# Performance work log

Hardware: AMD Instinct MI355X
Metric: run time of the kernel (lower is better)

## Reference

```python
import jax, jax.numpy as jnp
import numpy as np

B, L, S, D_MODEL, H = 2, 2048, 2048, 1024, 16
D_HEAD = D_MODEL // H  # 64


def setup_inputs() -> dict:
    key = jax.random.key(0)
    ks = jax.random.split(key, 11)
    s = 0.02
    return {
        "queries": jax.random.normal(ks[0], (B, L, D_MODEL), jnp.float32),
        "keys": jax.random.normal(ks[1], (B, S, D_MODEL), jnp.float32),
        "values": jax.random.normal(ks[2], (B, S, D_MODEL), jnp.float32),
        # Linear weights stored as [in, out] (torch W.T), biases [out]
        "Wq": jax.random.normal(ks[3], (D_MODEL, H * D_HEAD), jnp.float32) * s,
        "bq": jnp.zeros((H * D_HEAD,), jnp.float32),
        "Wk": jax.random.normal(ks[4], (D_MODEL, H * D_HEAD), jnp.float32) * s,
        "bk": jnp.zeros((H * D_HEAD,), jnp.float32),
        "Wv": jax.random.normal(ks[5], (D_MODEL, H * D_HEAD), jnp.float32) * s,
        "bv": jnp.zeros((H * D_HEAD,), jnp.float32),
        "Wo": jax.random.normal(ks[6], (H * D_HEAD, D_MODEL), jnp.float32) * s,
        "bo": jnp.zeros((D_MODEL,), jnp.float32),
    }


def reference(queries, keys, values, Wq, bq, Wk, bk, Wv, bv, Wo, bo):
    b, l, _ = queries.shape
    _, s, _ = keys.shape
    # QKV projections -> [B, L/S, H, D_HEAD]
    q = (queries @ Wq + bq).reshape(b, l, H, D_HEAD)
    k = (keys @ Wk + bk).reshape(b, s, H, D_HEAD)
    v = (values @ Wv + bv).reshape(b, s, H, D_HEAD)
    scale = 1.0 / jnp.sqrt(jnp.asarray(D_HEAD, q.dtype))
    # Full score matrix [B, H, L, S] (mask_flag=False -> no causal mask)
    scores = jnp.einsum("blhe,bshe->bhls", q, k)
    A = jax.nn.softmax(scale * scores, axis=-1)  # dropout is identity at eval
    out = jnp.einsum("bhls,bshd->blhd", A, v).reshape(b, l, H * D_HEAD)
    out = out @ Wo + bo
    return out, A
```

## Files before the change

### kernel.cpp

```cpp
#include <hip/hip_runtime.h>


typedef __attribute__((ext_vector_type(8))) __bf16 bf16x8;
typedef __attribute__((ext_vector_type(4))) float f32x4;

__device__ __forceinline__ unsigned int f2bf_u(float f) {
  unsigned int u = __float_as_uint(f);
  return (u + 0x7FFFu + ((u >> 16) & 1u)) >> 16;
}
__device__ __forceinline__ float bf2f(unsigned int h) {
  return __uint_as_float(h << 16);
}
__device__ __forceinline__ unsigned int pack2(float lo, float hi) {
  return (f2bf_u(hi) << 16) | f2bf_u(lo);
}
__device__ __forceinline__ f32x4 mfma16(bf16x8 a, bf16x8 b, f32x4 c) {
  return __builtin_amdgcn_mfma_f32_16x16x32_bf16(a, b, c, 0, 0, 0);
}
__device__ __forceinline__ void gll16(const void* g, void* l) {
  __builtin_amdgcn_global_load_lds(
      (const __attribute__((address_space(1))) unsigned int*)g,
      (__attribute__((address_space(3))) unsigned int*)l, 16, 0, 0);
}

__global__ __launch_bounds__(256) void transpose_w(
    const float* __restrict__ W0, const float* __restrict__ W1,
    const float* __restrict__ W2, const float* __restrict__ W3,
    unsigned short* __restrict__ T0, unsigned short* __restrict__ T1,
    unsigned short* __restrict__ T2, unsigned short* __restrict__ T3) {
  const float* W; unsigned short* T;
  switch (blockIdx.z) {
    case 0: W = W0; T = T0; break;
    case 1: W = W1; T = T1; break;
    case 2: W = W2; T = T2; break;
    default: W = W3; T = T3; break;
  }
  __shared__ float tile[32][33];
  const int tx = threadIdx.x, ty = threadIdx.y;
  const int i0 = blockIdx.x * 32, o0 = blockIdx.y * 32;
  #pragma unroll
  for (int r = 0; r < 4; ++r)
    tile[ty + 8 * r][tx] = W[(size_t)(i0 + ty + 8 * r) * 1024 + o0 + tx];
  __syncthreads();
  #pragma unroll
  for (int r = 0; r < 4; ++r)
    T[(size_t)(o0 + ty + 8 * r) * 1024 + i0 + tx] =
        (unsigned short)f2bf_u(tile[tx][ty + 8 * r]);
}

struct GemmJob {
  const float* A;
  const unsigned short* BT;
  const float* bias;
  void* C;
  int omode;
};
struct GemmJobs { GemmJob j[3]; };

__global__ __launch_bounds__(256) void gemm_qkv(GemmJobs jobs, int M, int N, int K) {
  const GemmJob jb = jobs.j[blockIdx.z];
  __shared__ unsigned short As[128][40];
  __shared__ unsigned short Bs[128][32];
  const int tid = threadIdx.x;
  const int lane = tid & 63, wid = tid >> 6;
  const int l15 = lane & 15, l4 = lane >> 4;
  const int m0 = blockIdx.x * 128, n0 = blockIdx.y * 128;
  const int wr = wid >> 1, wc = wid & 1;

  f32x4 acc[4][4];
  #pragma unroll
  for (int i = 0; i < 4; ++i)
    #pragma unroll
    for (int j = 0; j < 4; ++j) acc[i][j] = (f32x4){0.f, 0.f, 0.f, 0.f};

  const int nk = K >> 5;
  for (int kt = 0; kt < nk; ++kt) {
    #pragma unroll
    for (int c = 0; c < 4; ++c) {
      const int chunk = c * 256 + tid;
      const int row = chunk >> 3, col4 = chunk & 7;
      const float4 f = *(const float4*)(jb.A +
                                        (size_t)(m0 + row) * K + kt * 32 + col4 * 4);
      ushort4 o;
      o.x = (unsigned short)f2bf_u(f.x);
      o.y = (unsigned short)f2bf_u(f.y);
      o.z = (unsigned short)f2bf_u(f.z);
      o.w = (unsigned short)f2bf_u(f.w);
      *(ushort4*)&As[row][col4 * 4] = o;
    }
    #pragma unroll
    for (int c = 0; c < 2; ++c) {
      const int off = wid * 2048 + c * 1024;
      const int loff = off + lane * 16;
      const int row = loff >> 6, colb = loff & 63;
      gll16(jb.BT + (size_t)(n0 + row) * K + kt * 32 + colb / 2,
            (char*)&Bs[0][0] + off);
    }
    __syncthreads();
    bf16x8 af[4], bfr[4];
    #pragma unroll
    for (int i = 0; i < 4; ++i)
      af[i] = *(const bf16x8*)&As[wr * 64 + i * 16 + l15][l4 * 8];
    #pragma unroll
    for (int j = 0; j < 4; ++j)
      bfr[j] = *(const bf16x8*)&Bs[wc * 64 + j * 16 + l15][l4 * 8];
    #pragma unroll
    for (int i = 0; i < 4; ++i)
      #pragma unroll
      for (int j = 0; j < 4; ++j)
        acc[i][j] = mfma16(af[i], bfr[j], acc[i][j]);
    __syncthreads();
  }

  #pragma unroll
  for (int j = 0; j < 4; ++j) {
    const int col = n0 + wc * 64 + j * 16 + l15;
    const float bv = jb.bias[col];
    #pragma unroll
    for (int i = 0; i < 4; ++i) {
      const int rowb = m0 + wr * 64 + i * 16 + l4 * 4;
      if (jb.omode == 2) {
        const int bq = rowb >> 11, sq = rowb & 2047;
        const int hq = col >> 6, dq = col & 63;
        ushort4 o;
        o.x = (unsigned short)f2bf_u(acc[i][j][0] + bv);
        o.y = (unsigned short)f2bf_u(acc[i][j][1] + bv);
        o.z = (unsigned short)f2bf_u(acc[i][j][2] + bv);
        o.w = (unsigned short)f2bf_u(acc[i][j][3] + bv);
        *(ushort4*)((unsigned short*)jb.C +
                    ((size_t)((bq * 16 + hq) * 64 + dq) << 11) + sq) = o;
      } else {
        #pragma unroll
        for (int q = 0; q < 4; ++q)
          ((unsigned short*)jb.C)[(size_t)(rowb + q) * N + col] =
              (unsigned short)f2bf_u(acc[i][j][q] + bv);
      }
    }
  }
}

__global__ __launch_bounds__(256) void gemm_out(
    const unsigned short* __restrict__ Ap, const unsigned short* __restrict__ BT,
    const float* __restrict__ bias, float* __restrict__ Cp,
    int M, int N, int K) {
  __shared__ unsigned short As[128][32];
  __shared__ unsigned short Bs[64][32];
  const int tid = threadIdx.x;
  const int lane = tid & 63, w = tid >> 6;
  const int l15 = lane & 15, l4 = lane >> 4;
  const int m0 = blockIdx.x * 128, n0 = blockIdx.y * 64;

  f32x4 acc[2][4];
  #pragma unroll
  for (int i = 0; i < 2; ++i)
    #pragma unroll
    for (int j = 0; j < 4; ++j) acc[i][j] = (f32x4){0.f, 0.f, 0.f, 0.f};

  const int nk = K >> 5;
  for (int kt = 0; kt < nk; ++kt) {
    #pragma unroll
    for (int c = 0; c < 2; ++c) {
      const int off = (w * 2 + c) * 1024;
      const int loff = off + lane * 16;
      const int row = loff >> 6, colb = loff & 63;
      gll16(Ap + (size_t)(m0 + row) * K + kt * 32 + colb / 2,
            (char*)&As[0][0] + off);
    }
    {
      const int off = w * 1024;
      const int loff = off + lane * 16;
      const int row = loff >> 6, colb = loff & 63;
      gll16(BT + (size_t)(n0 + row) * K + kt * 32 + colb / 2,
            (char*)&Bs[0][0] + off);
    }
    __syncthreads();
    bf16x8 af[2], bfr[4];
    #pragma unroll
    for (int i = 0; i < 2; ++i)
      af[i] = *(const bf16x8*)&As[w * 32 + i * 16 + l15][l4 * 8];
    #pragma unroll
    for (int j = 0; j < 4; ++j)
      bfr[j] = *(const bf16x8*)&Bs[j * 16 + l15][l4 * 8];
    #pragma unroll
    for (int i = 0; i < 2; ++i)
      #pragma unroll
      for (int j = 0; j < 4; ++j)
        acc[i][j] = mfma16(af[i], bfr[j], acc[i][j]);
    __syncthreads();
  }

  #pragma unroll
  for (int j = 0; j < 4; ++j) {
    const int col = n0 + j * 16 + l15;
    const float bv = bias[col];
    #pragma unroll
    for (int i = 0; i < 2; ++i) {
      const int rowb = m0 + w * 32 + i * 16 + l4 * 4;
      #pragma unroll
      for (int q = 0; q < 4; ++q)
        Cp[(size_t)(rowb + q) * N + col] = acc[i][j][q] + bv;
    }
  }
}

__global__ __launch_bounds__(256) void attn_pv(
    const unsigned short* __restrict__ Q, const unsigned short* __restrict__ K,
    const unsigned short* __restrict__ VT, float2* __restrict__ Mst,
    unsigned short* __restrict__ OutPre) {
  __shared__ unsigned short Kt[128][64];
  __shared__ unsigned short Vt[64][128];

  const int tid = threadIdx.x;
  const int w = tid >> 6, lane = tid & 63;
  const int l15 = lane & 15, l4 = lane >> 4;
  const int wgid = blockIdx.x;
  const int xcd = wgid & 7, j = wgid >> 3;
  const int bh = xcd * 4 + (j >> 4);
  const int b = bh >> 4, h = bh & 15;
  const int m0 = (j & 15) * 128;
  const int base = w * 32;

  bf16x8 qf0[2], qf1[2];
  #pragma unroll
  for (int f = 0; f < 2; ++f) {
    const unsigned short* Qp =
        Q + ((size_t)(b * 2048 + m0 + base + f * 16 + l15) << 10) + h * 64 + l4 * 8;
    qf0[f] = *(const bf16x8*)Qp;
    qf1[f] = *(const bf16x8*)(Qp + 32);
  }

  const unsigned short* Kb = K + ((size_t)b << 21) + h * 64;
  const unsigned short* Vbh = VT + ((size_t)bh << 17);

  const int krow = lane >> 3;
  const int kcolb = (lane & 7) ^ krow;
  const int vrow = lane >> 4;

  float m_run[2] = {-3.0e38f, -3.0e38f};
  float l_run[2] = {0.f, 0.f};
  f32x4 pv[2][4];
  #pragma unroll
  for (int f = 0; f < 2; ++f)
    #pragma unroll
    for (int nt = 0; nt < 4; ++nt) pv[f][nt] = (f32x4){0.f, 0.f, 0.f, 0.f};

  for (int t = 0; t < 16; ++t) {
    #pragma unroll
    for (int c = 0; c < 4; ++c) {
      const int r = base + c * 8 + krow;
      gll16(Kb + ((size_t)(t * 128 + r) << 10) + kcolb * 8,
            &Kt[base + c * 8][0]);
    }
    #pragma unroll
    for (int c = 0; c < 4; ++c) {
      const int d = w * 16 + c * 4 + vrow;
      const int vc = (lane & 15) ^ (d & 7);
      gll16(Vbh + ((size_t)d << 11) + t * 128 + vc * 8,
            &Vt[w * 16 + c * 4][0]);
    }
    __syncthreads();

    unsigned int sc16[2][16];
    float tmax[2] = {-3.0e38f, -3.0e38f};
    #pragma unroll
    for (int sub = 0; sub < 8; ++sub) {
      const int row = sub * 16 + l15;
      const bf16x8 k0 = *(const bf16x8*)&Kt[row][(l4 ^ (l15 & 7)) * 8];
      const bf16x8 k1 = *(const bf16x8*)&Kt[row][((l4 + 4) ^ (l15 & 7)) * 8];
      #pragma unroll
      for (int f = 0; f < 2; ++f) {
        f32x4 a = {0.f, 0.f, 0.f, 0.f};
        a = mfma16(k0, qf0[f], a);
        a = mfma16(k1, qf1[f], a);
        const unsigned int u0 = f2bf_u(a[0] * 0.125f);
        const unsigned int u1 = f2bf_u(a[1] * 0.125f);
        const unsigned int u2 = f2bf_u(a[2] * 0.125f);
        const unsigned int u3 = f2bf_u(a[3] * 0.125f);
        sc16[f][sub * 2 + 0] = (u1 << 16) | u0;
        sc16[f][sub * 2 + 1] = (u3 << 16) | u2;
        tmax[f] = fmaxf(tmax[f], fmaxf(fmaxf(bf2f(u0), bf2f(u1)),
                                       fmaxf(bf2f(u2), bf2f(u3))));
      }
    }
    #pragma unroll
    for (int f = 0; f < 2; ++f) {
      float tm = tmax[f];
      tm = fmaxf(tm, __shfl_xor(tm, 16));
      tm = fmaxf(tm, __shfl_xor(tm, 32));
      const float m_new = fmaxf(m_run[f], tm);
      const float fs = __expf(m_run[f] - m_new);
      m_run[f] = m_new;
      float fr[4];
      #pragma unroll
      for (int r = 0; r < 4; ++r) fr[r] = __shfl(fs, l4 * 4 + r);
      #pragma unroll
      for (int nt = 0; nt < 4; ++nt) {
        pv[f][nt][0] *= fr[0]; pv[f][nt][1] *= fr[1];
        pv[f][nt][2] *= fr[2]; pv[f][nt][3] *= fr[3];
      }
      l_run[f] *= fs;
    }

    union EF { unsigned int u4[4]; bf16x8 v; } ef[2][4];
    #pragma unroll
    for (int f = 0; f < 2; ++f)
      #pragma unroll
      for (int kc = 0; kc < 4; ++kc)
        #pragma unroll
        for (int half = 0; half < 2; ++half) {
          const unsigned int p0 = sc16[f][(kc * 2 + half) * 2 + 0];
          const unsigned int p1 = sc16[f][(kc * 2 + half) * 2 + 1];
          const float e0 = __expf(bf2f(p0 & 0xffffu) - m_run[f]);
          const float e1 = __expf(bf2f(p0 >> 16) - m_run[f]);
          const float e2 = __expf(bf2f(p1 & 0xffffu) - m_run[f]);
          const float e3 = __expf(bf2f(p1 >> 16) - m_run[f]);
          l_run[f] += e0 + e1 + e2 + e3;
          ef[f][kc].u4[half * 2 + 0] = pack2(e0, e1);
          ef[f][kc].u4[half * 2 + 1] = pack2(e2, e3);
        }

    #pragma unroll
    for (int nt = 0; nt < 4; ++nt) {
      const int d = nt * 16 + l15;
      #pragma unroll
      for (int kc = 0; kc < 4; ++kc) {
        const int c16a = (kc * 4 + (l4 >> 1)) ^ (d & 7);
        const int c16b = (kc * 4 + 2 + (l4 >> 1)) ^ (d & 7);
        union { unsigned int u4[4]; bf16x8 v; } vf;
        const uint2 va = *(const uint2*)&Vt[d][c16a * 8 + (l4 & 1) * 4];
        const uint2 vb = *(const uint2*)&Vt[d][c16b * 8 + (l4 & 1) * 4];
        vf.u4[0] = va.x; vf.u4[1] = va.y; vf.u4[2] = vb.x; vf.u4[3] = vb.y;
        pv[0][nt] = mfma16(ef[0][kc].v, vf.v, pv[0][nt]);
        pv[1][nt] = mfma16(ef[1][kc].v, vf.v, pv[1][nt]);
      }
    }
    __syncthreads();
  }

  float linv[2];
  #pragma unroll
  for (int f = 0; f < 2; ++f) {
    float ls = l_run[f];
    ls += __shfl_xor(ls, 16);
    ls += __shfl_xor(ls, 32);
    linv[f] = 1.0f / ls;
  }
  if (lane < 16) {
    Mst[(size_t)bh * 2048 + m0 + base + lane] = make_float2(m_run[0], linv[0]);
    Mst[(size_t)bh * 2048 + m0 + base + 16 + lane] =
        make_float2(m_run[1], linv[1]);
  }
  #pragma unroll
  for (int f = 0; f < 2; ++f)
    #pragma unroll
    for (int r = 0; r < 4; ++r) {
      const float lq = __shfl(linv[f], l4 * 4 + r);
      const size_t rowoff =
          ((size_t)(b * 2048 + m0 + base + f * 16 + l4 * 4 + r) << 10) + h * 64;
      #pragma unroll
      for (int nt = 0; nt < 4; ++nt)
        OutPre[rowoff + nt * 16 + l15] =
            (unsigned short)f2bf_u(pv[f][nt][r] * lq);
    }
}

__global__ __launch_bounds__(512) void attn_awrite(
    const unsigned short* __restrict__ Q, const unsigned short* __restrict__ K,
    const float2* __restrict__ Mst, float* __restrict__ Aout) {
  __shared__ float atile[16][136];
  const int tid = threadIdx.x;
  const int w = tid >> 6, lane = tid & 63;
  const int l15 = lane & 15, l4 = lane >> 4;
  const int wgid = blockIdx.x;
  const int xcd = wgid & 7, j = wgid >> 3;
  const int bh = xcd * 4 + (j >> 7);
  const int b = bh >> 4, h = bh & 15;
  const int m0 = (j & 127) * 16;

  const unsigned short* Qp =
      Q + ((size_t)(b * 2048 + m0 + l15) << 10) + h * 64 + l4 * 8;
  const bf16x8 qf0 = *(const bf16x8*)Qp;
  const bf16x8 qf1 = *(const bf16x8*)(Qp + 32);
  const unsigned short* Kb = K + ((size_t)b << 21) + h * 64;

  const float2 ml = Mst[(size_t)bh * 2048 + m0 + l15];
  const float mreg = ml.x, lreg = ml.y;

  float* Awg = Aout + ((size_t)bh << 22) + ((size_t)m0 << 11);
  const int frow = tid >> 5;
  const int fcol = (tid & 31) * 4;

  const unsigned short* kp0 = Kb + ((size_t)(w * 16 + l15) << 10) + l4 * 8;
  bf16x8 ck0 = *(const bf16x8*)kp0;
  bf16x8 ck1 = *(const bf16x8*)(kp0 + 32);
  #pragma unroll
  for (int i = 0; i < 16; ++i) {
    bf16x8 nk0, nk1;
    if (i < 15) {
      const unsigned short* kp =
          Kb + ((size_t)((i + 1) * 128 + w * 16 + l15) << 10) + l4 * 8;
      nk0 = *(const bf16x8*)kp;
      nk1 = *(const bf16x8*)(kp + 32);
    }
    f32x4 a = {0.f, 0.f, 0.f, 0.f};
    a = mfma16(ck0, qf0, a);
    a = mfma16(ck1, qf1, a);
    ck0 = nk0;
    ck1 = nk1;
    f32x4 av;
    #pragma unroll
    for (int q = 0; q < 4; ++q) {
      const float sb = bf2f(f2bf_u(a[q] * 0.125f));
      av[q] = __expf(sb - mreg) * lreg;
    }
    *(f32x4*)&atile[l15][w * 16 + l4 * 4] = av;
    __syncthreads();
    const f32x4 v = *(const f32x4*)&atile[frow][fcol];
    __builtin_nontemporal_store(
        v, (f32x4*)(Awg + ((size_t)frow << 11) + i * 128 + fcol));
    __syncthreads();
  }
}

extern "C" void kernel_launch(void* const* d_in, const int* in_sizes, int n_in,
                              void* d_out, int out_size, void* d_ws,
                              size_t ws_size, hipStream_t stream) {
  (void)in_sizes; (void)n_in; (void)out_size; (void)ws_size;
  const float* queries = (const float*)d_in[0];
  const float* keys    = (const float*)d_in[1];
  const float* values  = (const float*)d_in[2];
  const float* Wq = (const float*)d_in[3];  const float* bq = (const float*)d_in[4];
  const float* Wk = (const float*)d_in[5];  const float* bk = (const float*)d_in[6];
  const float* Wv = (const float*)d_in[7];  const float* bv = (const float*)d_in[8];
  const float* Wo = (const float*)d_in[9];  const float* bo = (const float*)d_in[10];

  float* out  = (float*)d_out;
  float* Aout = out + (size_t)2 * 2048 * 1024;

  char* ws = (char*)d_ws;
  unsigned short* WqT = (unsigned short*)(ws + 0);
  unsigned short* WkT = (unsigned short*)(ws + 2097152);
  unsigned short* WvT = (unsigned short*)(ws + 4194304);
  unsigned short* WoT = (unsigned short*)(ws + 6291456);
  unsigned short* Qb  = (unsigned short*)(ws + 8388608);
  unsigned short* Kbf = (unsigned short*)(ws + 16777216);
  unsigned short* VTb = (unsigned short*)(ws + 25165824);
  unsigned short* Op  = (unsigned short*)(ws + 33554432);
  float2* Mst = (float2*)(ws + 41943040);

  transpose_w<<<dim3(32, 32, 4), dim3(32, 8), 0, stream>>>(
      Wq, Wk, Wv, Wo, WqT, WkT, WvT, WoT);

  GemmJobs qkv;
  qkv.j[0] = {queries, WqT, bq, Qb, 0};
  qkv.j[1] = {keys,    WkT, bk, Kbf, 0};
  qkv.j[2] = {values,  WvT, bv, VTb, 2};
  gemm_qkv<<<dim3(32, 8, 3), 256, 0, stream>>>(qkv, 4096, 1024, 1024);

  attn_pv<<<dim3(512), 256, 0, stream>>>(Qb, Kbf, VTb, Mst, Op);
  attn_awrite<<<dim3(4096), 512, 0, stream>>>(Qb, Kbf, Mst, Aout);

  gemm_out<<<dim3(32, 16), 256, 0, stream>>>(
      Op, WoT, bo, out, 4096, 1024, 1024);
}
```

Baseline: 294.5 us.

## Pre-convert QKV activations to bf16 and use async-LDS bf16 GEMM

```diff
diff --git a/kernel.cpp b/kernel.cpp
--- a/kernel.cpp
+++ b/kernel.cpp
@@ -46,6 +46,31 @@
   for (int r = 0; r < 4; ++r)
     T[(size_t)(o0 + ty + 8 * r) * 1024 + i0 + tx] =
         (unsigned short)f2bf_u(tile[tx][ty + 8 * r]);
+}
+
+__global__ __launch_bounds__(256) void convert_x(
+    const float* __restrict__ X0, const float* __restrict__ X1,
+    const float* __restrict__ X2,
+    unsigned short* __restrict__ Y0, unsigned short* __restrict__ Y1,
+    unsigned short* __restrict__ Y2) {
+  const float* X; unsigned short* Y;
+  switch (blockIdx.y) {
+    case 0: X = X0; Y = Y0; break;
+    case 1: X = X1; Y = Y1; break;
+    default: X = X2; Y = Y2; break;
+  }
+  const int idx = blockIdx.x * 256 + threadIdx.x;
+  #pragma unroll
+  for (int g = 0; g < 4; ++g) {
+    const size_t i = (size_t)idx + (size_t)g * 262144;
+    const float4 f = *(const float4*)(X + i * 4);
+    ushort4 o;
+    o.x = (unsigned short)f2bf_u(f.x);
+    o.y = (unsigned short)f2bf_u(f.y);
+    o.z = (unsigned short)f2bf_u(f.z);
+    o.w = (unsigned short)f2bf_u(f.w);
+    *(ushort4*)(Y + i * 4) = o;
+  }
 }
 
 struct GemmJob {
@@ -139,6 +164,92 @@
   }
 }
 
+struct GemmJobB {
+  const unsigned short* A;
+  const unsigned short* BT;
+  const float* bias;
+  void* C;
+  int omode;
+};
+struct GemmJobsB { GemmJobB j[3]; };
+
+__global__ __launch_bounds__(256) void gemm_qkv_bf16(GemmJobsB jobs, int M, int N, int K) {
+  const GemmJobB jb = jobs.j[blockIdx.z];
+  __shared__ unsigned short As[128][32];
+  __shared__ unsigned short Bs[128][32];
+  const int tid = threadIdx.x;
+  const int lane = tid & 63, wid = tid >> 6;
+  const int l15 = lane & 15, l4 = lane >> 4;
+  const int m0 = blockIdx.x * 128, n0 = blockIdx.y * 128;
+  const int wr = wid >> 1, wc = wid & 1;
+
+  f32x4 acc[4][4];
+  #pragma unroll
+  for (int i = 0; i < 4; ++i)
+    #pragma unroll
+    for (int j = 0; j < 4; ++j) acc[i][j] = (f32x4){0.f, 0.f, 0.f, 0.f};
+
+  const int nk = K >> 5;
+  for (int kt = 0; kt < nk; ++kt) {
+    #pragma unroll
+    for (int c = 0; c < 2; ++c) {
+      const int off = wid * 2048 + c * 1024;
+      const int loff = off + lane * 16;
+      const int row = loff >> 6, colb = loff & 63;
+      gll16(jb.A + (size_t)(m0 + row) * K + kt * 32 + colb / 2,
+            (char*)&As[0][0] + off);
+    }
+    #pragma unroll
+    for (int c = 0; c < 2; ++c) {
+      const int off = wid * 2048 + c * 1024;
+      const int loff = off + lane * 16;
+      const int row = loff >> 6, colb = loff & 63;
+      gll16(jb.BT + (size_t)(n0 + row) * K + kt * 32 + colb / 2,
+            (char*)&Bs[0][0] + off);
+    }
+    __syncthreads();
+    bf16x8 af[4], bfr[4];
+    #pragma unroll
+    for (int i = 0; i < 4; ++i)
+      af[i] = *(const bf16x8*)&As[wr * 64 + i * 16 + l15][l4 * 8];
+    #pragma unroll
+    for (int j = 0; j < 4; ++j)
+      bfr[j] = *(const bf16x8*)&Bs[wc * 64 + j * 16 + l15][l4 * 8];
+    #pragma unroll
+    for (int i = 0; i < 4; ++i)
+      #pragma unroll
+      for (int j = 0; j < 4; ++j)
+        acc[i][j] = mfma16(af[i], bfr[j], acc[i][j]);
+    __syncthreads();
+  }
+
+  #pragma unroll
+  for (int j = 0; j < 4; ++j) {
+    const int col = n0 + wc * 64 + j * 16 + l15;
+    const float bv = jb.bias[col];
+    #pragma unroll
+    for (int i = 0; i < 4; ++i) {
+      const int rowb = m0 + wr * 64 + i * 16 + l4 * 4;
+      if (jb.omode == 2) {
+        const int bq = rowb >> 11, sq = rowb & 2047;
+        const int hq = col >> 6, dq = col & 63;
+        ushort4 o;
+        o.x = (unsigned short)f2bf_u(acc[i][j][0] + bv);
+        o.y = (unsigned short)f2bf_u(acc[i][j][1] + bv);
+        o.z = (unsigned short)f2bf_u(acc[i][j][2] + bv);
+        o.w = (unsigned short)f2bf_u(acc[i][j][3] + bv);
+        *(ushort4*)((unsigned short*)jb.C +
+                    ((size_t)((bq * 16 + hq) * 64 + dq) << 11) + sq) = o;
+      } else {
+        #pragma unroll
+        for (int q = 0; q < 4; ++q)
+          ((unsigned short*)jb.C)[(size_t)(rowb + q) * N + col] =
+              (unsigned short)f2bf_u(acc[i][j][q] + bv);
+      }
+    }
+  }
+}
+
 __global__ __launch_bounds__(256) void gemm_out(
     const unsigned short* __restrict__ Ap, const unsigned short* __restrict__ BT,
     const float* __restrict__ bias, float* __restrict__ Cp,
@@ -425,7 +536,7 @@
 extern "C" void kernel_launch(void* const* d_in, const int* in_sizes, int n_in,
                               void* d_out, int out_size, void* d_ws,
                               size_t ws_size, hipStream_t stream) {
-  (void)in_sizes; (void)n_in; (void)out_size; (void)ws_size;
+  (void)in_sizes; (void)n_in; (void)out_size;
   const float* queries = (const float*)d_in[0];
   const float* keys    = (const float*)d_in[1];
   const float* values  = (const float*)d_in[2];
@@ -451,11 +562,24 @@
   transpose_w<<<dim3(32, 32, 4), dim3(32, 8), 0, stream>>>(
       Wq, Wk, Wv, Wo, WqT, WkT, WvT, WoT);
 
-  GemmJobs qkv;
-  qkv.j[0] = {queries, WqT, bq, Qb, 0};
-  qkv.j[1] = {keys,    WkT, bk, Kbf, 0};
-  qkv.j[2] = {values,  WvT, bv, VTb, 2};
-  gemm_qkv<<<dim3(32, 8, 3), 256, 0, stream>>>(qkv, 4096, 1024, 1024);
+  const size_t NEED = 59244544;
+  if (ws_size >= NEED) {
+    unsigned short* Qc = (unsigned short*)(ws + 42467328);
+    unsigned short* Kc = (unsigned short*)(ws + 50855936);
+    unsigned short* Vc = (unsigned short*)(ws + 33554432);
+    convert_x<<<dim3(1024, 3), 256, 0, stream>>>(queries, keys, values, Qc, Kc, Vc);
+    GemmJobsB qkv;
+    qkv.j[0] = {Qc, WqT, bq, Qb, 0};
+    qkv.j[1] = {Kc, WkT, bk, Kbf, 0};
+    qkv.j[2] = {Vc, WvT, bv, VTb, 2};
+    gemm_qkv_bf16<<<dim3(32, 8, 3), 256, 0, stream>>>(qkv, 4096, 1024, 1024);
+  } else {
+    GemmJobs qkv;
+    qkv.j[0] = {queries, WqT, bq, Qb, 0};
+    qkv.j[1] = {keys,    WkT, bk, Kbf, 0};
+    qkv.j[2] = {values,  WvT, bv, VTb, 2};
+    gemm_qkv<<<dim3(32, 8, 3), 256, 0, stream>>>(qkv, 4096, 1024, 1024);
+  }
 
   attn_pv<<<dim3(512), 256, 0, stream>>>(Qb, Kbf, VTb, Mst, Op);
   attn_awrite<<<dim3(4096), 512, 0, stream>>>(Qb, Kbf, Mst, Aout);
```

Measured after the change: 300.9 us. 2.2% more time.
